# Optimization experiments

Hardware: AMD Instinct MI355X
Metric: run time of the kernel (lower is better)

## Reference

```python
import jax, jax.numpy as jnp
import numpy as np

N_HEAD = 16
D_MODEL = 1024
D_K = 64
D_V = 64
LN_EPS = 1e-6


def setup_inputs() -> dict:
    key = jax.random.key(0)
    ks = jax.random.split(key, 10)
    B, S = 2, 2048
    scale = 0.02
    return {
        "q": jax.random.normal(ks[0], (B, S, D_MODEL), jnp.float32),
        "k": jax.random.normal(ks[1], (B, S, D_MODEL), jnp.float32),
        "v": jax.random.normal(ks[2], (B, S, D_MODEL), jnp.float32),
        "Wq": jax.random.normal(ks[3], (D_MODEL, N_HEAD * D_K), jnp.float32) * scale,
        "Wk": jax.random.normal(ks[4], (D_MODEL, N_HEAD * D_K), jnp.float32) * scale,
        "Wv": jax.random.normal(ks[5], (D_MODEL, N_HEAD * D_V), jnp.float32) * scale,
        "Wfc": jax.random.normal(ks[6], (N_HEAD * D_V, D_MODEL), jnp.float32) * scale,
        "bfc": jnp.zeros((D_MODEL,), jnp.float32),
        "gamma": jnp.ones((D_MODEL,), jnp.float32),
        "beta": jnp.zeros((D_MODEL,), jnp.float32),
    }


def reference(q, k, v, Wq, Wk, Wv, Wfc, bfc, gamma, beta):
    B, S, _ = q.shape
    residual = q
    # QKV projections, split into heads: [B, S, H, Dh]
    qh = (q @ Wq).reshape(B, S, N_HEAD, D_K)
    kh = (k @ Wk).reshape(B, S, N_HEAD, D_K)
    vh = (v @ Wv).reshape(B, S, N_HEAD, D_V)
    # scaled dot-product attention (explicit score matrix, as in source)
    temperature = jnp.asarray(D_K, qh.dtype) ** 0.5
    attn = jnp.einsum("bqhd,bkhd->bhqk", qh, kh) / temperature
    attn = jax.nn.softmax(attn, axis=-1)
    out = jnp.einsum("bhqk,bkhd->bqhd", attn, vh).reshape(B, S, N_HEAD * D_V)
    # output projection (dropout is identity in eval mode)
    out = out @ Wfc + bfc
    # residual + layernorm (eps=1e-6)
    x = out + residual
    mu = jnp.mean(x, axis=-1, keepdims=True)
    var = jnp.mean(jnp.square(x - mu), axis=-1, keepdims=True)
    return (x - mu) / jnp.sqrt(var + LN_EPS) * gamma + beta
```

## Files before the change

kernel.cpp:

```cpp
#include <hip/hip_runtime.h>

typedef float f32x4 __attribute__((ext_vector_type(4)));
typedef short short8 __attribute__((ext_vector_type(8)));
typedef unsigned short ushort_t;

#define D_MODEL 1024
#define N_HEAD 16
#define D_K 64
#define SEQ 2048
#define BATCH 2
#define M_TOK 4096
#define HD 1024
#define QSCALE 0.125f

__device__ __forceinline__ ushort_t f2bf(float f) {
    union { float f; unsigned int u; } x; x.f = f;
    unsigned int r = x.u + 0x7fffu + ((x.u >> 16) & 1u);
    return (ushort_t)(r >> 16);
}
__device__ __forceinline__ ushort_t f2bf_fast(float f) {
    union { float f; unsigned int u; } x; x.f = f;
    return (ushort_t)((x.u + 0x8000u) >> 16);
}

__device__ __forceinline__ void async_copy16(const ushort_t* gptr, ushort_t* lptr) {
    __builtin_amdgcn_global_load_lds(
        (const __attribute__((address_space(1))) unsigned int*)gptr,
        (__attribute__((address_space(3))) unsigned int*)lptr, 16, 0, 0);
}

__global__ __launch_bounds__(256) void transpose_cast(const float* __restrict__ in,
                                                      ushort_t* __restrict__ out,
                                                      int R, int C) {
    __shared__ ushort_t t[32][33];
    int bc = blockIdx.x * 32, br = blockIdx.y * 32;
    for (int i = threadIdx.y; i < 32; i += 8)
        t[i][threadIdx.x] = f2bf(in[(size_t)(br + i) * C + bc + threadIdx.x]);
    __syncthreads();
    for (int i = threadIdx.y; i < 32; i += 8)
        out[(size_t)(bc + i) * R + br + threadIdx.x] = t[threadIdx.x][i];
}

__global__ __launch_bounds__(256) void transpose_bf16(const ushort_t* __restrict__ in,
                                                      ushort_t* __restrict__ out,
                                                      int R, int C) {
    __shared__ ushort_t t[32][33];
    int bc = blockIdx.x * 32, br = blockIdx.y * 32;
    for (int i = threadIdx.y; i < 32; i += 8)
        t[i][threadIdx.x] = in[(size_t)(br + i) * C + bc + threadIdx.x];
    __syncthreads();
    for (int i = threadIdx.y; i < 32; i += 8)
        out[(size_t)(bc + i) * R + br + threadIdx.x] = t[threadIdx.x][i];
}

__global__ __launch_bounds__(256) void cast_bf16_3(const float* __restrict__ q,
                                                   const float* __restrict__ k,
                                                   const float* __restrict__ v,
                                                   ushort_t* __restrict__ qo,
                                                   ushort_t* __restrict__ ko,
                                                   ushort_t* __restrict__ vo) {
    int z = blockIdx.z;
    const float* s = (z == 0) ? q : (z == 1) ? k : v;
    ushort_t* d = (z == 0) ? qo : (z == 1) ? ko : vo;
    size_t i = ((size_t)blockIdx.x * 256 + threadIdx.x) * 8;
    float4 a = *(const float4*)(s + i);
    float4 b = *(const float4*)(s + i + 4);
    ushort_t tmp[8] = {f2bf(a.x), f2bf(a.y), f2bf(a.z), f2bf(a.w),
                       f2bf(b.x), f2bf(b.y), f2bf(b.z), f2bf(b.w)};
    *(short8*)(d + i) = *(short8*)tmp;
}

__global__ __launch_bounds__(256) void gemm_qkv(const ushort_t* __restrict__ qb,
                                                const ushort_t* __restrict__ kb,
                                                const ushort_t* __restrict__ vb,
                                                const ushort_t* __restrict__ wq,
                                                const ushort_t* __restrict__ wk,
                                                const ushort_t* __restrict__ wv,
                                                ushort_t* __restrict__ Qo,
                                                ushort_t* __restrict__ Ko,
                                                ushort_t* __restrict__ Vo) {
    __shared__ ushort_t As[128 * 32];
    __shared__ ushort_t Bs[128 * 32];
    const int z = blockIdx.z;
    const ushort_t* A = (z == 0) ? qb : (z == 1) ? kb : vb;
    const ushort_t* Bt = (z == 0) ? wq : (z == 1) ? wk : wv;
    ushort_t* C = (z == 0) ? Qo : (z == 1) ? Ko : Vo;
    const float scale = (z == 0) ? QSCALE : 1.0f;
    const int tid = threadIdx.x;
    const int wave = tid >> 6, lane = tid & 63;
    const int quad = lane >> 4, l16 = lane & 15;
    const int m0 = blockIdx.y * 128, n0 = blockIdx.x * 128;
    const int wm = (wave >> 1) * 64, wn = (wave & 1) * 64;
    const int K = D_MODEL, N = D_MODEL;

    f32x4 acc[4][4];
    for (int i = 0; i < 4; ++i)
        for (int j = 0; j < 4; ++j) acc[i][j] = (f32x4){0.f, 0.f, 0.f, 0.f};

    for (int kk = 0; kk < K; kk += 32) {
        __syncthreads();
        #pragma unroll
        for (int c = 0; c < 2; ++c) {
            int flat = ((wave * 2 + c) * 64 + lane) * 8;
            int r = flat >> 5, col = flat & 31;
            async_copy16(Bt + (size_t)(n0 + r) * K + kk + col, &Bs[(wave * 2 + c) * 512]);
            async_copy16(A + (size_t)(m0 + r) * K + kk + col, &As[(wave * 2 + c) * 512]);
        }
        __syncthreads();
        short8 af[4], bfr[4];
        #pragma unroll
        for (int i = 0; i < 4; ++i)
            af[i] = *(const short8*)&As[(wm + i * 16 + l16) * 32 + quad * 8];
        #pragma unroll
        for (int j = 0; j < 4; ++j)
            bfr[j] = *(const short8*)&Bs[(wn + j * 16 + l16) * 32 + quad * 8];
        #pragma unroll
        for (int i = 0; i < 4; ++i)
            #pragma unroll
            for (int j = 0; j < 4; ++j)
                acc[i][j] = __builtin_amdgcn_mfma_f32_16x16x32_bf16(af[i], bfr[j], acc[i][j], 0, 0, 0);
    }
    #pragma unroll
    for (int i = 0; i < 4; ++i)
        #pragma unroll
        for (int j = 0; j < 4; ++j) {
            int n = n0 + wn + j * 16 + l16;
            #pragma unroll
            for (int r = 0; r < 4; ++r) {
                int m = m0 + wm + i * 16 + quad * 4 + r;
                C[(size_t)m * N + n] = f2bf(acc[i][j][r] * scale);
            }
        }
}

__global__ __launch_bounds__(256) void gemm_fc(const ushort_t* __restrict__ A,
                                               const ushort_t* __restrict__ Bt,
                                               float* __restrict__ Cf,
                                               const float* __restrict__ bias,
                                               const float* __restrict__ resid) {
    __shared__ ushort_t As[128 * 32];
    __shared__ ushort_t Bs[128 * 32];
    const int tid = threadIdx.x;
    const int wave = tid >> 6, lane = tid & 63;
    const int quad = lane >> 4, l16 = lane & 15;
    const int m0 = blockIdx.y * 128, n0 = blockIdx.x * 128;
    const int wm = (wave >> 1) * 64, wn = (wave & 1) * 64;
    const int K = D_MODEL, N = D_MODEL;

    f32x4 acc[4][4];
    for (int i = 0; i < 4; ++i)
        for (int j = 0; j < 4; ++j) acc[i][j] = (f32x4){0.f, 0.f, 0.f, 0.f};

    for (int kk = 0; kk < K; kk += 32) {
        __syncthreads();
        #pragma unroll
        for (int c = 0; c < 2; ++c) {
            int flat = ((wave * 2 + c) * 64 + lane) * 8;
            int r = flat >> 5, col = flat & 31;
            async_copy16(Bt + (size_t)(n0 + r) * K + kk + col, &Bs[(wave * 2 + c) * 512]);
            async_copy16(A + (size_t)(m0 + r) * K + kk + col, &As[(wave * 2 + c) * 512]);
        }
        __syncthreads();
        short8 af[4], bfr[4];
        #pragma unroll
        for (int i = 0; i < 4; ++i)
            af[i] = *(const short8*)&As[(wm + i * 16 + l16) * 32 + quad * 8];
        #pragma unroll
        for (int j = 0; j < 4; ++j)
            bfr[j] = *(const short8*)&Bs[(wn + j * 16 + l16) * 32 + quad * 8];
        #pragma unroll
        for (int i = 0; i < 4; ++i)
            #pragma unroll
            for (int j = 0; j < 4; ++j)
                acc[i][j] = __builtin_amdgcn_mfma_f32_16x16x32_bf16(af[i], bfr[j], acc[i][j], 0, 0, 0);
    }
    #pragma unroll
    for (int i = 0; i < 4; ++i)
        #pragma unroll
        for (int j = 0; j < 4; ++j) {
            int n = n0 + wn + j * 16 + l16;
            #pragma unroll
            for (int r = 0; r < 4; ++r) {
                int m = m0 + wm + i * 16 + quad * 4 + r;
                Cf[(size_t)m * N + n] = acc[i][j][r] + bias[n] + resid[(size_t)m * N + n];
            }
        }
}

__global__ __launch_bounds__(256) void attn64(const ushort_t* __restrict__ Qh,
                                              const ushort_t* __restrict__ Kh,
                                              const ushort_t* __restrict__ Vt,
                                              ushort_t* __restrict__ O) {
    __shared__ ushort_t Ks[2 * 64 * 32];
    __shared__ ushort_t Vs[2 * 64 * 32];
    __shared__ ushort_t Ps[4 * 16 * 72];
    const int tid = threadIdx.x;
    const int wave = tid >> 6, lane = tid & 63;
    const int quad = lane >> 4, l16 = lane & 15;
    const int b = blockIdx.z, h = blockIdx.y, qt = blockIdx.x;
    const size_t base = (size_t)b * SEQ * HD + h * 64;
    const ushort_t* Qb = Qh + base + (size_t)(qt * 64) * HD;
    const ushort_t* Kb = Kh + base;
    const ushort_t* Vb = Vt + (size_t)(h * 64) * M_TOK + (size_t)b * SEQ;

    short8 qf[2];
    {
        int qr = wave * 16 + l16;
        #pragma unroll
        for (int s = 0; s < 2; ++s)
            qf[s] = *(const short8*)(Qb + (size_t)qr * HD + s * 32 + quad * 8);
    }
    f32x4 oacc[4];
    float lsum[4] = {0.f, 0.f, 0.f, 0.f};
    #pragma unroll
    for (int vt = 0; vt < 4; ++vt) oacc[vt] = (f32x4){0.f, 0.f, 0.f, 0.f};

    ushort_t* Pw = &Ps[wave * 16 * 72];

    for (int kt = 0; kt < SEQ / 64; ++kt) {
        __syncthreads();
        #pragma unroll
        for (int c = 0; c < 2; ++c) {
            int g = wave * 2 + c;
            int sH = g >> 2, row = (g & 3) * 16 + (lane >> 2), e = (lane & 3) * 8;
            async_copy16(Kb + (size_t)(kt * 64 + row) * HD + sH * 32 + e, &Ks[g * 512]);
            async_copy16(Vb + (size_t)row * M_TOK + kt * 64 + sH * 32 + e, &Vs[g * 512]);
        }
        __syncthreads();

        f32x4 sacc[4];
        #pragma unroll
        for (int nt = 0; nt < 4; ++nt) sacc[nt] = (f32x4){0.f, 0.f, 0.f, 0.f};
        #pragma unroll
        for (int s = 0; s < 2; ++s)
            #pragma unroll
            for (int nt = 0; nt < 4; ++nt) {
                short8 kf = *(const short8*)&Ks[s * 2048 + (nt * 16 + l16) * 32 + quad * 8];
                sacc[nt] = __builtin_amdgcn_mfma_f32_16x16x32_bf16(qf[s], kf, sacc[nt], 0, 0, 0);
            }

        #pragma unroll
        for (int nt = 0; nt < 4; ++nt)
            #pragma unroll
            for (int r = 0; r < 4; ++r) {
                float pv = __expf(sacc[nt][r]);
                lsum[r] += pv;
                Pw[(quad * 4 + r) * 72 + nt * 16 + l16] = f2bf_fast(pv);
            }

        #pragma unroll
        for (int s = 0; s < 2; ++s) {
            short8 pf = *(const short8*)&Pw[l16 * 72 + s * 32 + quad * 8];
            #pragma unroll
            for (int vt = 0; vt < 4; ++vt) {
                short8 vf = *(const short8*)&Vs[s * 2048 + (vt * 16 + l16) * 32 + quad * 8];
                oacc[vt] = __builtin_amdgcn_mfma_f32_16x16x32_bf16(pf, vf, oacc[vt], 0, 0, 0);
            }
        }
    }
    #pragma unroll
    for (int off = 1; off < 16; off <<= 1)
        #pragma unroll
        for (int r = 0; r < 4; ++r) lsum[r] += __shfl_xor(lsum[r], off, 64);

    ushort_t* Ob = O + base + (size_t)(qt * 64) * HD;
    #pragma unroll
    for (int r = 0; r < 4; ++r) {
        float inv = 1.f / lsum[r];
        int row = wave * 16 + quad * 4 + r;
        #pragma unroll
        for (int vt = 0; vt < 4; ++vt)
            Ob[(size_t)row * HD + vt * 16 + l16] = f2bf(oacc[vt][r] * inv);
    }
}

__global__ __launch_bounds__(256) void ln_kernel(float* __restrict__ x,
                                                 const float* __restrict__ gamma,
                                                 const float* __restrict__ beta) {
    const int D = D_MODEL;
    float* xr = x + (size_t)blockIdx.x * D;
    const int tid = threadIdx.x;
    float4 v = *(const float4*)(xr + tid * 4);
    float s = v.x + v.y + v.z + v.w;
    float s2 = v.x * v.x + v.y * v.y + v.z * v.z + v.w * v.w;
    #pragma unroll
    for (int off = 1; off < 64; off <<= 1) {
        s += __shfl_xor(s, off, 64);
        s2 += __shfl_xor(s2, off, 64);
    }
    __shared__ float ws1[4], ws2[4];
    int wave = tid >> 6, lane = tid & 63;
    if (lane == 0) { ws1[wave] = s; ws2[wave] = s2; }
    __syncthreads();
    s = ws1[0] + ws1[1] + ws1[2] + ws1[3];
    s2 = ws2[0] + ws2[1] + ws2[2] + ws2[3];
    float mean = s * (1.f / D);
    float var = s2 * (1.f / D) - mean * mean;
    float rstd = rsqrtf(var + 1e-6f);
    float4 g = *(const float4*)(gamma + tid * 4);
    float4 bt = *(const float4*)(beta + tid * 4);
    float4 o;
    o.x = (v.x - mean) * rstd * g.x + bt.x;
    o.y = (v.y - mean) * rstd * g.y + bt.y;
    o.z = (v.z - mean) * rstd * g.z + bt.z;
    o.w = (v.w - mean) * rstd * g.w + bt.w;
    *(float4*)(xr + tid * 4) = o;
}

extern "C" void kernel_launch(void* const* d_in, const int* in_sizes, int n_in,
                              void* d_out, int out_size, void* d_ws, size_t ws_size,
                              hipStream_t stream) {
    const float* q = (const float*)d_in[0];
    const float* k = (const float*)d_in[1];
    const float* v = (const float*)d_in[2];
    const float* Wq = (const float*)d_in[3];
    const float* Wk = (const float*)d_in[4];
    const float* Wv = (const float*)d_in[5];
    const float* Wfc = (const float*)d_in[6];
    const float* bfc = (const float*)d_in[7];
    const float* gamma = (const float*)d_in[8];
    const float* beta = (const float*)d_in[9];
    float* out = (float*)d_out;

    char* ws = (char*)d_ws;
    const size_t MB = 1u << 20;
    ushort_t* WqT  = (ushort_t*)(ws + 0 * MB);
    ushort_t* WkT  = (ushort_t*)(ws + 2 * MB);
    ushort_t* WvT  = (ushort_t*)(ws + 4 * MB);
    ushort_t* WfcT = (ushort_t*)(ws + 6 * MB);
    ushort_t* qb   = (ushort_t*)(ws + 8 * MB);
    ushort_t* kb   = (ushort_t*)(ws + 16 * MB);
    ushort_t* vb   = (ushort_t*)(ws + 24 * MB);
    ushort_t* Qh   = (ushort_t*)(ws + 32 * MB);
    ushort_t* Kh   = (ushort_t*)(ws + 40 * MB);
    ushort_t* Vh   = (ushort_t*)(ws + 48 * MB);
    ushort_t* Oh   = (ushort_t*)(ws + 8 * MB);
    ushort_t* Vt   = (ushort_t*)(ws + 16 * MB);

    const int M = M_TOK, D = D_MODEL;
    dim3 tb(32, 8);
    transpose_cast<<<dim3(D / 32, D / 32), tb, 0, stream>>>(Wq, WqT, D, D);
    transpose_cast<<<dim3(D / 32, D / 32), tb, 0, stream>>>(Wk, WkT, D, D);
    transpose_cast<<<dim3(D / 32, D / 32), tb, 0, stream>>>(Wv, WvT, D, D);
    transpose_cast<<<dim3(D / 32, D / 32), tb, 0, stream>>>(Wfc, WfcT, D, D);

    cast_bf16_3<<<dim3(M * D / (256 * 8), 1, 3), 256, 0, stream>>>(q, k, v, qb, kb, vb);

    gemm_qkv<<<dim3(D / 128, M / 128, 3), 256, 0, stream>>>(qb, kb, vb, WqT, WkT, WvT, Qh, Kh, Vh);

    transpose_bf16<<<dim3(D / 32, M / 32), tb, 0, stream>>>(Vh, Vt, M, D);

    attn64<<<dim3(SEQ / 64, N_HEAD, BATCH), 256, 0, stream>>>(Qh, Kh, Vt, Oh);

    gemm_fc<<<dim3(D / 128, M / 128), 256, 0, stream>>>(Oh, WfcT, out, bfc, q);

    ln_kernel<<<M, 256, 0, stream>>>(out, gamma, beta);
}
```

Measured before the change: 272.5 us.

## Fuse V transpose into QKV GEMM, double-buffer attention, MFMA row sums

```diff
diff --git a/kernel.cpp b/kernel.cpp
--- a/kernel.cpp
+++ b/kernel.cpp
@@ -2,16 +2,16 @@
 
 typedef float f32x4 __attribute__((ext_vector_type(4)));
 typedef short short8 __attribute__((ext_vector_type(8)));
+typedef short short4v __attribute__((ext_vector_type(4)));
 typedef unsigned short ushort_t;
 
 #define D_MODEL 1024
 #define N_HEAD 16
-#define D_K 64
 #define SEQ 2048
 #define BATCH 2
 #define M_TOK 4096
 #define HD 1024
-#define QSCALE 0.125f
+#define QSCALE_L2E 0.1803368801111f
 
 __device__ __forceinline__ ushort_t f2bf(float f) {
     union { float f; unsigned int u; } x; x.f = f;
@@ -29,25 +29,22 @@
         (__attribute__((address_space(3))) unsigned int*)lptr, 16, 0, 0);
 }
 
-__global__ __launch_bounds__(256) void transpose_cast(const float* __restrict__ in,
-                                                      ushort_t* __restrict__ out,
-                                                      int R, int C) {
+__global__ __launch_bounds__(256) void transpose_cast4(const float* __restrict__ w0,
+                                                       const float* __restrict__ w1,
+                                                       const float* __restrict__ w2,
+                                                       const float* __restrict__ w3,
+                                                       ushort_t* __restrict__ o0,
+                                                       ushort_t* __restrict__ o1,
+                                                       ushort_t* __restrict__ o2,
+                                                       ushort_t* __restrict__ o3) {
+    const int R = D_MODEL, C = D_MODEL;
+    int z = blockIdx.z;
+    const float* in = (z == 0) ? w0 : (z == 1) ? w1 : (z == 2) ? w2 : w3;
+    ushort_t* out = (z == 0) ? o0 : (z == 1) ? o1 : (z == 2) ? o2 : o3;
     __shared__ ushort_t t[32][33];
     int bc = blockIdx.x * 32, br = blockIdx.y * 32;
     for (int i = threadIdx.y; i < 32; i += 8)
         t[i][threadIdx.x] = f2bf(in[(size_t)(br + i) * C + bc + threadIdx.x]);
-    __syncthreads();
-    for (int i = threadIdx.y; i < 32; i += 8)
-        out[(size_t)(bc + i) * R + br + threadIdx.x] = t[threadIdx.x][i];
-}
-
-__global__ __launch_bounds__(256) void transpose_bf16(const ushort_t* __restrict__ in,
-                                                      ushort_t* __restrict__ out,
-                                                      int R, int C) {
-    __shared__ ushort_t t[32][33];
-    int bc = blockIdx.x * 32, br = blockIdx.y * 32;
-    for (int i = threadIdx.y; i < 32; i += 8)
-        t[i][threadIdx.x] = in[(size_t)(br + i) * C + bc + threadIdx.x];
     __syncthreads();
     for (int i = threadIdx.y; i < 32; i += 8)
         out[(size_t)(bc + i) * R + br + threadIdx.x] = t[threadIdx.x][i];
@@ -78,14 +75,12 @@
                                                 const ushort_t* __restrict__ wv,
                                                 ushort_t* __restrict__ Qo,
                                                 ushort_t* __restrict__ Ko,
-                                                ushort_t* __restrict__ Vo) {
+                                                ushort_t* __restrict__ VtO) {
     __shared__ ushort_t As[128 * 32];
     __shared__ ushort_t Bs[128 * 32];
     const int z = blockIdx.z;
     const ushort_t* A = (z == 0) ? qb : (z == 1) ? kb : vb;
     const ushort_t* Bt = (z == 0) ? wq : (z == 1) ? wk : wv;
-    ushort_t* C = (z == 0) ? Qo : (z == 1) ? Ko : Vo;
-    const float scale = (z == 0) ? QSCALE : 1.0f;
     const int tid = threadIdx.x;
     const int wave = tid >> 6, lane = tid & 63;
     const int quad = lane >> 4, l16 = lane & 15;
@@ -120,17 +115,33 @@
             for (int j = 0; j < 4; ++j)
                 acc[i][j] = __builtin_amdgcn_mfma_f32_16x16x32_bf16(af[i], bfr[j], acc[i][j], 0, 0, 0);
     }
-    #pragma unroll
-    for (int i = 0; i < 4; ++i)
-        #pragma unroll
-        for (int j = 0; j < 4; ++j) {
-            int n = n0 + wn + j * 16 + l16;
-            #pragma unroll
-            for (int r = 0; r < 4; ++r) {
-                int m = m0 + wm + i * 16 + quad * 4 + r;
-                C[(size_t)m * N + n] = f2bf(acc[i][j][r] * scale);
-            }
-        }
+    if (z == 2) {
+        #pragma unroll
+        for (int i = 0; i < 4; ++i)
+            #pragma unroll
+            for (int j = 0; j < 4; ++j) {
+                int n = n0 + wn + j * 16 + l16;
+                int m = m0 + wm + i * 16 + quad * 4;
+                ushort_t tmp[4];
+                #pragma unroll
+                for (int r = 0; r < 4; ++r) tmp[r] = f2bf(acc[i][j][r]);
+                *(short4v*)&VtO[(size_t)n * M_TOK + m] = *(short4v*)tmp;
+            }
+    } else {
+        ushort_t* C = (z == 0) ? Qo : Ko;
+        const float scale = (z == 0) ? QSCALE_L2E : 1.0f;
+        #pragma unroll
+        for (int i = 0; i < 4; ++i)
+            #pragma unroll
+            for (int j = 0; j < 4; ++j) {
+                int n = n0 + wn + j * 16 + l16;
+                #pragma unroll
+                for (int r = 0; r < 4; ++r) {
+                    int m = m0 + wm + i * 16 + quad * 4 + r;
+                    C[(size_t)m * N + n] = f2bf(acc[i][j][r] * scale);
+                }
+            }
+    }
 }
 
 __global__ __launch_bounds__(256) void gemm_fc(const ushort_t* __restrict__ A,
@@ -191,9 +202,9 @@
                                               const ushort_t* __restrict__ Kh,
                                               const ushort_t* __restrict__ Vt,
                                               ushort_t* __restrict__ O) {
-    __shared__ ushort_t Ks[2 * 64 * 32];
-    __shared__ ushort_t Vs[2 * 64 * 32];
-    __shared__ ushort_t Ps[4 * 16 * 72];
+    __shared__ ushort_t Ks[2][64 * 64];
+    __shared__ ushort_t Vs[2][64 * 64];
+    __shared__ ushort_t Ps[4][16 * 72];
     const int tid = threadIdx.x;
     const int wave = tid >> 6, lane = tid & 63;
     const int quad = lane >> 4, l16 = lane & 15;
@@ -210,23 +221,29 @@
         for (int s = 0; s < 2; ++s)
             qf[s] = *(const short8*)(Qb + (size_t)qr * HD + s * 32 + quad * 8);
     }
+    const short8 ones = {16256, 16256, 16256, 16256, 16256, 16256, 16256, 16256};
     f32x4 oacc[4];
-    float lsum[4] = {0.f, 0.f, 0.f, 0.f};
+    f32x4 lacc = (f32x4){0.f, 0.f, 0.f, 0.f};
     #pragma unroll
     for (int vt = 0; vt < 4; ++vt) oacc[vt] = (f32x4){0.f, 0.f, 0.f, 0.f};
 
-    ushort_t* Pw = &Ps[wave * 16 * 72];
-
-    for (int kt = 0; kt < SEQ / 64; ++kt) {
-        __syncthreads();
+    ushort_t* Pw = Ps[wave];
+
+    auto stage = [&](int kt, int buf) {
         #pragma unroll
         for (int c = 0; c < 2; ++c) {
             int g = wave * 2 + c;
             int sH = g >> 2, row = (g & 3) * 16 + (lane >> 2), e = (lane & 3) * 8;
-            async_copy16(Kb + (size_t)(kt * 64 + row) * HD + sH * 32 + e, &Ks[g * 512]);
-            async_copy16(Vb + (size_t)row * M_TOK + kt * 64 + sH * 32 + e, &Vs[g * 512]);
-        }
-        __syncthreads();
+            async_copy16(Kb + (size_t)(kt * 64 + row) * HD + sH * 32 + e, &Ks[buf][g * 512]);
+            async_copy16(Vb + (size_t)row * M_TOK + kt * 64 + sH * 32 + e, &Vs[buf][g * 512]);
+        }
+    };
+
+    stage(0, 0);
+    for (int kt = 0; kt < SEQ / 64; ++kt) {
+        const int buf = kt & 1;
+        __syncthreads();
+        if (kt + 1 < SEQ / 64) stage(kt + 1, buf ^ 1);
 
         f32x4 sacc[4];
         #pragma unroll
@@ -235,7 +252,7 @@
         for (int s = 0; s < 2; ++s)
             #pragma unroll
             for (int nt = 0; nt < 4; ++nt) {
-                short8 kf = *(const short8*)&Ks[s * 2048 + (nt * 16 + l16) * 32 + quad * 8];
+                short8 kf = *(const short8*)&Ks[buf][s * 2048 + (nt * 16 + l16) * 32 + quad * 8];
                 sacc[nt] = __builtin_amdgcn_mfma_f32_16x16x32_bf16(qf[s], kf, sacc[nt], 0, 0, 0);
             }
 
@@ -243,30 +260,26 @@
         for (int nt = 0; nt < 4; ++nt)
             #pragma unroll
             for (int r = 0; r < 4; ++r) {
-                float pv = __expf(sacc[nt][r]);
-                lsum[r] += pv;
+                float pv = exp2f(sacc[nt][r]);
                 Pw[(quad * 4 + r) * 72 + nt * 16 + l16] = f2bf_fast(pv);
             }
 
         #pragma unroll
         for (int s = 0; s < 2; ++s) {
             short8 pf = *(const short8*)&Pw[l16 * 72 + s * 32 + quad * 8];
+            lacc = __builtin_amdgcn_mfma_f32_16x16x32_bf16(pf, ones, lacc, 0, 0, 0);
             #pragma unroll
             for (int vt = 0; vt < 4; ++vt) {
-                short8 vf = *(const short8*)&Vs[s * 2048 + (vt * 16 + l16) * 32 + quad * 8];
+                short8 vf = *(const short8*)&Vs[buf][s * 2048 + (vt * 16 + l16) * 32 + quad * 8];
                 oacc[vt] = __builtin_amdgcn_mfma_f32_16x16x32_bf16(pf, vf, oacc[vt], 0, 0, 0);
             }
         }
     }
-    #pragma unroll
-    for (int off = 1; off < 16; off <<= 1)
-        #pragma unroll
-        for (int r = 0; r < 4; ++r) lsum[r] += __shfl_xor(lsum[r], off, 64);
 
     ushort_t* Ob = O + base + (size_t)(qt * 64) * HD;
     #pragma unroll
     for (int r = 0; r < 4; ++r) {
-        float inv = 1.f / lsum[r];
+        float inv = 1.f / lacc[r];
         int row = wave * 16 + quad * 4 + r;
         #pragma unroll
         for (int vt = 0; vt < 4; ++vt)
@@ -333,22 +346,16 @@
     ushort_t* vb   = (ushort_t*)(ws + 24 * MB);
     ushort_t* Qh   = (ushort_t*)(ws + 32 * MB);
     ushort_t* Kh   = (ushort_t*)(ws + 40 * MB);
-    ushort_t* Vh   = (ushort_t*)(ws + 48 * MB);
+    ushort_t* Vt   = (ushort_t*)(ws + 48 * MB);
     ushort_t* Oh   = (ushort_t*)(ws + 8 * MB);
-    ushort_t* Vt   = (ushort_t*)(ws + 16 * MB);
 
     const int M = M_TOK, D = D_MODEL;
-    dim3 tb(32, 8);
-    transpose_cast<<<dim3(D / 32, D / 32), tb, 0, stream>>>(Wq, WqT, D, D);
-    transpose_cast<<<dim3(D / 32, D / 32), tb, 0, stream>>>(Wk, WkT, D, D);
-    transpose_cast<<<dim3(D / 32, D / 32), tb, 0, stream>>>(Wv, WvT, D, D);
-    transpose_cast<<<dim3(D / 32, D / 32), tb, 0, stream>>>(Wfc, WfcT, D, D);
+    transpose_cast4<<<dim3(D / 32, D / 32, 4), dim3(32, 8), 0, stream>>>(
+        Wq, Wk, Wv, Wfc, WqT, WkT, WvT, WfcT);
 
     cast_bf16_3<<<dim3(M * D / (256 * 8), 1, 3), 256, 0, stream>>>(q, k, v, qb, kb, vb);
 
-    gemm_qkv<<<dim3(D / 128, M / 128, 3), 256, 0, stream>>>(qb, kb, vb, WqT, WkT, WvT, Qh, Kh, Vh);
-
-    transpose_bf16<<<dim3(D / 32, M / 32), tb, 0, stream>>>(Vh, Vt, M, D);
+    gemm_qkv<<<dim3(D / 128, M / 128, 3), 256, 0, stream>>>(qb, kb, vb, WqT, WkT, WvT, Qh, Kh, Vt);
 
     attn64<<<dim3(SEQ / 64, N_HEAD, BATCH), 256, 0, stream>>>(Qh, Kh, Vt, Oh);
 
```

Measured after the change: 287.5 us. 5.5% more time.
